# Optimization experiments

Measured on AMD Instinct MI355X. Metric: run time of the kernel, lower is better.

The kernel has to match this reference:

```python
import jax, jax.numpy as jnp
import numpy as np

B, D = 32768, 256          # batch, latent_size
L, K = 4, 2048             # n_codebooks, codebook_size
BETA = 0.25                # commitment loss weight (EMA layer uses only beta term)


def setup_inputs() -> dict:
    key = jax.random.key(0)
    kx, kc = jax.random.split(key)
    x = jax.random.normal(kx, (B, D), dtype=jnp.float32)
    # per-level codebooks (EMAVQLayer.embed, xavier-normal-ish scale)
    codebooks = jax.random.normal(kc, (L, K, D), dtype=jnp.float32) * 0.1
    return {"x": x, "codebooks": codebooks}


def reference(x, codebooks):
    """RQLayer.forward (EMA variant, eval-path math; EMA buffer updates are
    side effects and do not change forward outputs)."""
    sg = jax.lax.stop_gradient
    quantized = jnp.zeros_like(x)
    loss = jnp.zeros((), x.dtype)
    unused = jnp.zeros((), jnp.int32)
    inds = []
    for l in range(L):  # small fixed number of residual levels
        c = codebooks[l]                                   # [K, D]
        dist = (jnp.sum(x * x, axis=1, keepdims=True)
                - 2.0 * (x @ c.T)
                + jnp.sum(c * c, axis=1)[None, :])
        ind = jnp.argmin(dist, axis=1)                     # [B]
        x_q = c[ind]                                       # gather [B, D]
        counts = jnp.zeros((K,), jnp.int32).at[ind].add(1)
        unused = unused + jnp.sum(counts == 0)
        loss = loss + BETA * jnp.mean((x - sg(x_q)) ** 2)
        quant = x + sg(x_q - x)                            # straight-through
        x = x - quant                                      # residual (== sg(x - x_q))
        quantized = quantized + quant
        inds.append(ind)
    return quantized, loss / L, unused, jnp.stack(inds, axis=1)
```

## Files before the change

### kernel.cpp

```cpp
#include <hip/hip_runtime.h>

#define NT 512
#define B_ 32768
#define D_ 256
#define L_ 4
#define K_ 2048
#define BM 64
#define NBLK (B_/BM)
#define BETA_ 0.25f

#define OUT_LOSS   8388608
#define OUT_UNUSED 8388609
#define OUT_INDS   8388610


__global__ __launch_bounds__(256) void rq_prep(const float* __restrict__ cb,
                                               int* __restrict__ counts,
                                               float* __restrict__ cnorm) {
  int cw = blockIdx.x * 256 + threadIdx.x;
  if (cw >= L_ * K_) return;
  counts[cw] = 0;
  const float4* cb4 = (const float4*)cb;
  float s = 0.f;
  for (int d4 = 0; d4 < 64; ++d4) {
    float4 v = cb4[(size_t)cw * 64 + d4];
    s = __fadd_rn(s, __fmul_rn(v.x, v.x));
    s = __fadd_rn(s, __fmul_rn(v.y, v.y));
    s = __fadd_rn(s, __fmul_rn(v.z, v.z));
    s = __fadd_rn(s, __fmul_rn(v.w, v.w));
  }
  cnorm[cw] = s;
}

__device__ __forceinline__ int cstp(int c) { return ((c & 7) << 3) | (c >> 3); }

template<int CTRL>
__device__ __forceinline__ float dpp_f(float v) {
  return __int_as_float(__builtin_amdgcn_update_dpp(0, __float_as_int(v), CTRL, 0xF, 0xF, true));
}
template<int CTRL>
__device__ __forceinline__ int dpp_i(int v) {
  return __builtin_amdgcn_update_dpp(0, v, CTRL, 0xF, 0xF, true);
}
#define XOR1 0xB1
#define XOR2 0x4E
#define XOR8 0x128

__global__ __attribute__((amdgpu_flat_work_group_size(NT, NT), amdgpu_waves_per_eu(1)))
void rq_main(
    const float* __restrict__ x, const float* __restrict__ cb,
    float* __restrict__ out, int* __restrict__ counts,
    const float* __restrict__ cnorm, float* __restrict__ lpart) {
  __shared__ float4 xs[64][64];
  __shared__ float4 cs[64][64];
  __shared__ float  red_v[8][64];
  __shared__ int    red_i[8][64];
  __shared__ float  xxs[64];
  __shared__ int    ind_s[64];
  __shared__ float  lred[NT];

  const int tid  = threadIdx.x;
  const int lane = tid & 63;
  const int wave = tid >> 6;
  const int dg   = (lane & 3) | ((lane >> 1) & 4);
  const int p    = ((lane >> 2) & 1) | ((lane >> 3) & 6);
  const int row0 = blockIdx.x * BM;
  const float4* x4  = (const float4*)x;
  const float4* cb4 = (const float4*)cb;

  const int sl  = cstp(lane);
  const int d4r = cstp(lane ^ wave);

  {
    float4 v[8];
    #pragma unroll
    for (int it = 0; it < 8; ++it)
      v[it] = x4[(size_t)(row0 + wave + (it << 3)) * 64 + d4r];
    #pragma unroll
    for (int it = 0; it < 8; ++it)
      xs[wave + (it << 3)][lane] = v[it];
  }

  float4 st[8];
  #pragma unroll
  for (int it = 0; it < 8; ++it)
    st[it] = cb4[(size_t)(wave * 8 + it) * 64 + sl];
  #pragma unroll
  for (int it = 0; it < 8; ++it)
    cs[wave * 8 + it][lane] = st[it];

  const float4* xsp[8];
  const float4* csp[8];
  #pragma unroll
  for (int i = 0; i < 8; ++i) xsp[i] = &xs[p * 8 + i][dg ^ i];
  #pragma unroll
  for (int j = 0; j < 8; ++j) csp[j] = &cs[wave * 8 + (j ^ dg)][dg];

  float lsum = 0.f;
  const int kb = (wave << 3) | dg;
  float4* out4 = (float4*)out;

  for (int l = 0; l < L_; ++l) {
    __syncthreads();

    if (tid < 64) {
      const int sr = tid & 7;
      float s = 0.f;
      for (int d4 = 0; d4 < 64; ++d4) {
        float4 v = xs[tid][cstp(d4) ^ sr];
        s = __fadd_rn(s, __fmul_rn(v.x, v.x));
        s = __fadd_rn(s, __fmul_rn(v.y, v.y));
        s = __fadd_rn(s, __fmul_rn(v.z, v.z));
        s = __fadd_rn(s, __fmul_rn(v.w, v.w));
      }
      xxs[tid] = s;
    }
    __syncthreads();

    float xxr[8];
    #pragma unroll
    for (int i = 0; i < 8; ++i) xxr[i] = xxs[p * 8 + i];

    float bv[8]; int bi[8];
    #pragma unroll
    for (int i = 0; i < 8; ++i) { bv[i] = 3.4e38f; bi[i] = 0; }
    const float* cnl = cnorm + l * K_;

    for (int ch = 0; ch < 32; ++ch) {
      {
        int tn = l * 32 + ch + 1; if (tn > 127) tn = 127;
        const float4* src = cb4 + (size_t)tn * 4096;
        #pragma unroll
        for (int it = 0; it < 8; ++it)
          st[it] = src[(size_t)(wave * 8 + it) * 64 + sl];
      }
      const float cn = cnl[(ch << 6) + kb];

      float acc[8][8];

      {
        float4 xv[8], cv[8];
        #pragma unroll
        for (int i = 0; i < 8; ++i) xv[i] = xsp[i][0];
        #pragma unroll
        for (int j = 0; j < 8; ++j) cv[j] = csp[j][0];
        #pragma unroll
        for (int i = 0; i < 8; ++i)
          #pragma unroll
          for (int j = 0; j < 8; ++j) {
            float a = __fmul_rn(xv[i].x, cv[j].x);
            a = fmaf(xv[i].y, cv[j].y, a);
            a = fmaf(xv[i].z, cv[j].z, a);
            a = fmaf(xv[i].w, cv[j].w, a);
            acc[i][j] = a;
          }
      }
      #pragma unroll
      for (int d = 1; d < 8; ++d) {
        float4 xv[8], cv[8];
        #pragma unroll
        for (int i = 0; i < 8; ++i) xv[i] = xsp[i][d << 3];
        #pragma unroll
        for (int j = 0; j < 8; ++j) cv[j] = csp[j][d << 3];
        #pragma unroll
        for (int i = 0; i < 8; ++i)
          #pragma unroll
          for (int j = 0; j < 8; ++j) {
            acc[i][j] = fmaf(xv[i].x, cv[j].x, acc[i][j]);
            acc[i][j] = fmaf(xv[i].y, cv[j].y, acc[i][j]);
            acc[i][j] = fmaf(xv[i].z, cv[j].z, acc[i][j]);
            acc[i][j] = fmaf(xv[i].w, cv[j].w, acc[i][j]);
          }
      }

      #pragma unroll
      for (int it = 0; it < 8; ++it)
        cs[wave * 8 + it][lane] = st[it];

      #pragma unroll
      for (int i = 0; i < 8; ++i) {
        acc[i][0] += dpp_f<XOR1>(acc[i][1]);
        acc[i][2] += dpp_f<XOR1>(acc[i][3]);
        acc[i][4] += dpp_f<XOR1>(acc[i][5]);
        acc[i][6] += dpp_f<XOR1>(acc[i][7]);
        acc[i][0] += dpp_f<XOR2>(acc[i][2]);
        acc[i][4] += dpp_f<XOR2>(acc[i][6]);
        acc[i][0] += dpp_f<XOR8>(acc[i][4]);
      }

      const int kidx = (ch << 6) + kb;
      #pragma unroll
      for (int i = 0; i < 8; ++i) {
        float s = __fadd_rn(__fsub_rn(xxr[i], __fmul_rn(2.0f, acc[i][0])), cn);
        if (s < bv[i]) { bv[i] = s; bi[i] = kidx; }
      }
    }

    #pragma unroll
    for (int i = 0; i < 8; ++i) {
      { float pv = dpp_f<XOR1>(bv[i]); int pi = dpp_i<XOR1>(bi[i]);
        if (pv < bv[i] || (pv == bv[i] && pi < bi[i])) { bv[i] = pv; bi[i] = pi; } }
      { float pv = dpp_f<XOR2>(bv[i]); int pi = dpp_i<XOR2>(bi[i]);
        if (pv < bv[i] || (pv == bv[i] && pi < bi[i])) { bv[i] = pv; bi[i] = pi; } }
      { float pv = dpp_f<XOR8>(bv[i]); int pi = dpp_i<XOR8>(bi[i]);
        if (pv < bv[i] || (pv == bv[i] && pi < bi[i])) { bv[i] = pv; bi[i] = pi; } }
    }
    if (dg == 0) {
      #pragma unroll
      for (int i = 0; i < 8; ++i) {
        red_v[wave][p * 8 + i] = bv[i];
        red_i[wave][p * 8 + i] = bi[i];
      }
    }
    __syncthreads();
    if (tid < 64) {
      float bv_ = red_v[0][tid]; int bi_ = red_i[0][tid];
      #pragma unroll
      for (int w = 1; w < 8; ++w) {
        float v = red_v[w][tid]; int ii = red_i[w][tid];
        if (v < bv_ || (v == bv_ && ii < bi_)) { bv_ = v; bi_ = ii; }
      }
      ind_s[tid] = bi_;
      out[(size_t)OUT_INDS + (size_t)(row0 + tid) * L_ + l] = (float)bi_;
      atomicAdd(&counts[l * K_ + bi_], 1);
    }
    __syncthreads();

    #pragma unroll
    for (int it = 0; it < 8; ++it) {
      const int r = wave + (it << 3);
      const size_t oidx = (size_t)(row0 + r) * 64 + d4r;
      float4 xv = xs[r][lane];
      float4 cv = cb4[(size_t)(l * K_ + ind_s[r]) * 64 + d4r];
      float tx = __fsub_rn(cv.x, xv.x); float qx = __fadd_rn(xv.x, tx); float nx = __fsub_rn(xv.x, qx);
      float ty = __fsub_rn(cv.y, xv.y); float qy = __fadd_rn(xv.y, ty); float ny = __fsub_rn(xv.y, qy);
      float tz = __fsub_rn(cv.z, xv.z); float qz = __fadd_rn(xv.z, tz); float nz = __fsub_rn(xv.z, qz);
      float tw = __fsub_rn(cv.w, xv.w); float qw = __fadd_rn(xv.w, tw); float nw = __fsub_rn(xv.w, qw);
      float4 prev = (l == 0) ? make_float4(0.f, 0.f, 0.f, 0.f) : out4[oidx];
      out4[oidx] = make_float4(__fadd_rn(prev.x, qx), __fadd_rn(prev.y, qy),
                               __fadd_rn(prev.z, qz), __fadd_rn(prev.w, qw));
      float ex = __fsub_rn(xv.x, cv.x);
      float ey = __fsub_rn(xv.y, cv.y);
      float ez = __fsub_rn(xv.z, cv.z);
      float ew = __fsub_rn(xv.w, cv.w);
      lsum = __fadd_rn(lsum, __fmul_rn(ex, ex));
      lsum = __fadd_rn(lsum, __fmul_rn(ey, ey));
      lsum = __fadd_rn(lsum, __fmul_rn(ez, ez));
      lsum = __fadd_rn(lsum, __fmul_rn(ew, ew));
      xs[r][lane] = make_float4(nx, ny, nz, nw);
    }
  }

  lred[tid] = lsum;
  __syncthreads();
  for (int s = NT / 2; s > 0; s >>= 1) {
    if (tid < s) lred[tid] += lred[tid + s];
    __syncthreads();
  }
  if (tid == 0) lpart[blockIdx.x] = lred[0];
}

__global__ __launch_bounds__(256) void rq_final(const int* __restrict__ counts,
                                                const float* __restrict__ lpart,
                                                float* __restrict__ out) {
  __shared__ double fs[256];
  __shared__ int    is_[256];
  int tid = threadIdx.x;
  double ls = 0.0;
  for (int i = tid; i < NBLK; i += 256) ls += (double)lpart[i];
  int uz = 0;
  for (int i = tid; i < L_ * K_; i += 256) uz += (counts[i] == 0) ? 1 : 0;
  fs[tid] = ls; is_[tid] = uz;
  __syncthreads();
  for (int s = 128; s > 0; s >>= 1) {
    if (tid < s) { fs[tid] += fs[tid + s]; is_[tid] += is_[tid + s]; }
    __syncthreads();
  }
  if (tid == 0) {
    out[OUT_LOSS]   = (float)(fs[0] * (double)BETA_ / ((double)B_ * (double)D_ * (double)L_));
    out[OUT_UNUSED] = (float)is_[0];
  }
}

extern "C" void kernel_launch(void* const* d_in, const int* in_sizes, int n_in,
                              void* d_out, int out_size, void* d_ws, size_t ws_size,
                              hipStream_t stream) {
  const float* x  = (const float*)d_in[0];
  const float* cb = (const float*)d_in[1];
  float* out = (float*)d_out;
  int*   counts = (int*)d_ws;
  float* cnorm  = (float*)((char*)d_ws + 32768);
  float* lpart  = (float*)((char*)d_ws + 65536);

  rq_prep<<<(L_ * K_ + 255) / 256, 256, 0, stream>>>(cb, counts, cnorm);
  rq_main<<<NBLK, NT, 0, stream>>>(x, cb, out, counts, cnorm, lpart);
  rq_final<<<1, 256, 0, stream>>>(counts, lpart, out);
}
```

Baseline: 1.882 ms.

## Repartition distance tile: 4 rows by 8 codes per thread, padded x tile

After: 1.927 ms. 2.4% more time.

```diff
diff --git a/kernel.cpp b/kernel.cpp
--- a/kernel.cpp
+++ b/kernel.cpp
@@ -32,8 +32,6 @@
   cnorm[cw] = s;
 }
 
-__device__ __forceinline__ int cstp(int c) { return ((c & 7) << 3) | (c >> 3); }
-
 template<int CTRL>
 __device__ __forceinline__ float dpp_f(float v) {
   return __int_as_float(__builtin_amdgcn_update_dpp(0, __float_as_int(v), CTRL, 0xF, 0xF, true));
@@ -44,14 +42,13 @@
 }
 #define XOR1 0xB1
 #define XOR2 0x4E
-#define XOR8 0x128
 
 __global__ __attribute__((amdgpu_flat_work_group_size(NT, NT), amdgpu_waves_per_eu(1)))
 void rq_main(
     const float* __restrict__ x, const float* __restrict__ cb,
     float* __restrict__ out, int* __restrict__ counts,
     const float* __restrict__ cnorm, float* __restrict__ lpart) {
-  __shared__ float4 xs[64][64];
+  __shared__ float4 xs[64][65];
   __shared__ float4 cs[64][64];
   __shared__ float  red_v[8][64];
   __shared__ int    red_i[8][64];
@@ -62,20 +59,17 @@
   const int tid  = threadIdx.x;
   const int lane = tid & 63;
   const int wave = tid >> 6;
-  const int dg   = (lane & 3) | ((lane >> 1) & 4);
-  const int p    = ((lane >> 2) & 1) | ((lane >> 3) & 6);
+  const int dg   = lane & 3;
+  const int p    = lane >> 2;
   const int row0 = blockIdx.x * BM;
   const float4* x4  = (const float4*)x;
   const float4* cb4 = (const float4*)cb;
 
-  const int sl  = cstp(lane);
-  const int d4r = cstp(lane ^ wave);
-
   {
     float4 v[8];
     #pragma unroll
     for (int it = 0; it < 8; ++it)
-      v[it] = x4[(size_t)(row0 + wave + (it << 3)) * 64 + d4r];
+      v[it] = x4[(size_t)(row0 + wave + (it << 3)) * 64 + lane];
     #pragma unroll
     for (int it = 0; it < 8; ++it)
       xs[wave + (it << 3)][lane] = v[it];
@@ -84,17 +78,15 @@
   float4 st[8];
   #pragma unroll
   for (int it = 0; it < 8; ++it)
-    st[it] = cb4[(size_t)(wave * 8 + it) * 64 + sl];
+    st[it] = cb4[(size_t)(wave * 8 + it) * 64 + lane];
   #pragma unroll
   for (int it = 0; it < 8; ++it)
     cs[wave * 8 + it][lane] = st[it];
 
-  const float4* xsp[8];
-  const float4* csp[8];
+  const float4* xb = &xs[p * 4][dg];
+  const float4* cvp[4];
   #pragma unroll
-  for (int i = 0; i < 8; ++i) xsp[i] = &xs[p * 8 + i][dg ^ i];
-  #pragma unroll
-  for (int j = 0; j < 8; ++j) csp[j] = &cs[wave * 8 + (j ^ dg)][dg];
+  for (int jj = 0; jj < 4; ++jj) cvp[jj] = &cs[wave * 8 + (jj ^ dg)][dg];
 
   float lsum = 0.f;
   const int kb = (wave << 3) | dg;
@@ -104,10 +96,9 @@
     __syncthreads();
 
     if (tid < 64) {
-      const int sr = tid & 7;
       float s = 0.f;
       for (int d4 = 0; d4 < 64; ++d4) {
-        float4 v = xs[tid][cstp(d4) ^ sr];
+        float4 v = xs[tid][d4];
         s = __fadd_rn(s, __fmul_rn(v.x, v.x));
         s = __fadd_rn(s, __fmul_rn(v.y, v.y));
         s = __fadd_rn(s, __fmul_rn(v.z, v.z));
@@ -117,13 +108,13 @@
     }
     __syncthreads();
 
-    float xxr[8];
-    #pragma unroll
-    for (int i = 0; i < 8; ++i) xxr[i] = xxs[p * 8 + i];
-
-    float bv[8]; int bi[8];
-    #pragma unroll
-    for (int i = 0; i < 8; ++i) { bv[i] = 3.4e38f; bi[i] = 0; }
+    float xxr[4];
+    #pragma unroll
+    for (int i = 0; i < 4; ++i) xxr[i] = xxs[p * 4 + i];
+
+    float bv[4]; int bi[4];
+    #pragma unroll
+    for (int i = 0; i < 4; ++i) { bv[i] = 3.4e38f; bi[i] = 0; }
     const float* cnl = cnorm + l * K_;
 
     for (int ch = 0; ch < 32; ++ch) {
@@ -132,20 +123,21 @@
         const float4* src = cb4 + (size_t)tn * 4096;
         #pragma unroll
         for (int it = 0; it < 8; ++it)
-          st[it] = src[(size_t)(wave * 8 + it) * 64 + sl];
-      }
-      const float cn = cnl[(ch << 6) + kb];
-
-      float acc[8][8];
+          st[it] = src[(size_t)(wave * 8 + it) * 64 + lane];
+      }
+      const float cn0 = cnl[(ch << 6) + kb];
+      const float cn4 = cnl[(ch << 6) + kb + 4];
+
+      float acc[4][8];
 
       {
-        float4 xv[8], cv[8];
-        #pragma unroll
-        for (int i = 0; i < 8; ++i) xv[i] = xsp[i][0];
-        #pragma unroll
-        for (int j = 0; j < 8; ++j) cv[j] = csp[j][0];
-        #pragma unroll
-        for (int i = 0; i < 8; ++i)
+        float4 xv[4], cv[8];
+        #pragma unroll
+        for (int i = 0; i < 4; ++i) xv[i] = xb[i * 65];
+        #pragma unroll
+        for (int j = 0; j < 4; ++j) { cv[j] = cvp[j][0]; cv[j + 4] = cvp[j][256]; }
+        #pragma unroll
+        for (int i = 0; i < 4; ++i)
           #pragma unroll
           for (int j = 0; j < 8; ++j) {
             float a = __fmul_rn(xv[i].x, cv[j].x);
@@ -156,14 +148,14 @@
           }
       }
       #pragma unroll
-      for (int d = 1; d < 8; ++d) {
-        float4 xv[8], cv[8];
-        #pragma unroll
-        for (int i = 0; i < 8; ++i) xv[i] = xsp[i][d << 3];
-        #pragma unroll
-        for (int j = 0; j < 8; ++j) cv[j] = csp[j][d << 3];
-        #pragma unroll
-        for (int i = 0; i < 8; ++i)
+      for (int t = 1; t < 16; ++t) {
+        float4 xv[4], cv[8];
+        #pragma unroll
+        for (int i = 0; i < 4; ++i) xv[i] = xb[i * 65 + t * 4];
+        #pragma unroll
+        for (int j = 0; j < 4; ++j) { cv[j] = cvp[j][t * 4]; cv[j + 4] = cvp[j][t * 4 + 256]; }
+        #pragma unroll
+        for (int i = 0; i < 4; ++i)
           #pragma unroll
           for (int j = 0; j < 8; ++j) {
             acc[i][j] = fmaf(xv[i].x, cv[j].x, acc[i][j]);
@@ -178,38 +170,37 @@
         cs[wave * 8 + it][lane] = st[it];
 
       #pragma unroll
-      for (int i = 0; i < 8; ++i) {
+      for (int i = 0; i < 4; ++i) {
         acc[i][0] += dpp_f<XOR1>(acc[i][1]);
         acc[i][2] += dpp_f<XOR1>(acc[i][3]);
+        acc[i][0] += dpp_f<XOR2>(acc[i][2]);
         acc[i][4] += dpp_f<XOR1>(acc[i][5]);
         acc[i][6] += dpp_f<XOR1>(acc[i][7]);
-        acc[i][0] += dpp_f<XOR2>(acc[i][2]);
         acc[i][4] += dpp_f<XOR2>(acc[i][6]);
-        acc[i][0] += dpp_f<XOR8>(acc[i][4]);
       }
 
       const int kidx = (ch << 6) + kb;
       #pragma unroll
-      for (int i = 0; i < 8; ++i) {
-        float s = __fadd_rn(__fsub_rn(xxr[i], __fmul_rn(2.0f, acc[i][0])), cn);
-        if (s < bv[i]) { bv[i] = s; bi[i] = kidx; }
-      }
-    }
-
-    #pragma unroll
-    for (int i = 0; i < 8; ++i) {
+      for (int i = 0; i < 4; ++i) {
+        float s0 = __fadd_rn(__fsub_rn(xxr[i], __fmul_rn(2.0f, acc[i][0])), cn0);
+        if (s0 < bv[i]) { bv[i] = s0; bi[i] = kidx; }
+        float s4 = __fadd_rn(__fsub_rn(xxr[i], __fmul_rn(2.0f, acc[i][4])), cn4);
+        if (s4 < bv[i]) { bv[i] = s4; bi[i] = kidx + 4; }
+      }
+    }
+
+    #pragma unroll
+    for (int i = 0; i < 4; ++i) {
       { float pv = dpp_f<XOR1>(bv[i]); int pi = dpp_i<XOR1>(bi[i]);
         if (pv < bv[i] || (pv == bv[i] && pi < bi[i])) { bv[i] = pv; bi[i] = pi; } }
       { float pv = dpp_f<XOR2>(bv[i]); int pi = dpp_i<XOR2>(bi[i]);
         if (pv < bv[i] || (pv == bv[i] && pi < bi[i])) { bv[i] = pv; bi[i] = pi; } }
-      { float pv = dpp_f<XOR8>(bv[i]); int pi = dpp_i<XOR8>(bi[i]);
-        if (pv < bv[i] || (pv == bv[i] && pi < bi[i])) { bv[i] = pv; bi[i] = pi; } }
     }
     if (dg == 0) {
       #pragma unroll
-      for (int i = 0; i < 8; ++i) {
-        red_v[wave][p * 8 + i] = bv[i];
-        red_i[wave][p * 8 + i] = bi[i];
+      for (int i = 0; i < 4; ++i) {
+        red_v[wave][p * 4 + i] = bv[i];
+        red_i[wave][p * 4 + i] = bi[i];
       }
     }
     __syncthreads();
@@ -229,9 +220,9 @@
     #pragma unroll
     for (int it = 0; it < 8; ++it) {
       const int r = wave + (it << 3);
-      const size_t oidx = (size_t)(row0 + r) * 64 + d4r;
+      const size_t oidx = (size_t)(row0 + r) * 64 + lane;
       float4 xv = xs[r][lane];
-      float4 cv = cb4[(size_t)(l * K_ + ind_s[r]) * 64 + d4r];
+      float4 cv = cb4[(size_t)(l * K_ + ind_s[r]) * 64 + lane];
       float tx = __fsub_rn(cv.x, xv.x); float qx = __fadd_rn(xv.x, tx); float nx = __fsub_rn(xv.x, qx);
       float ty = __fsub_rn(cv.y, xv.y); float qy = __fadd_rn(xv.y, ty); float ny = __fsub_rn(xv.y, qy);
       float tz = __fsub_rn(cv.z, xv.z); float qz = __fadd_rn(xv.z, tz); float nz = __fsub_rn(xv.z, qz);
```
